# Optimization experiments

Hardware: AMD Instinct MI355X
Metric: run time of the kernel (lower is better)

The kernel has to match this reference:

```python
import jax, jax.numpy as jnp
import numpy as np

E, H = 1024, 16
N, S, T = 2, 2048, 2048


def setup_inputs() -> dict:
    key = jax.random.key(0)
    ks = jax.random.split(key, 8)
    scale = 1.0 / np.sqrt(E)
    q = jax.random.normal(ks[0], (N, S, E), dtype=jnp.float32)
    k = jax.random.normal(ks[1], (N, T, E), dtype=jnp.float32)
    v = jax.random.normal(ks[2], (N, T, E), dtype=jnp.float32)
    pad_mask = jax.random.randint(ks[3], (N, 1, 1, T), 0, 2, dtype=jnp.int32)
    subsq_mask = jnp.tril(jnp.ones((S, T), dtype=jnp.int32))[None, None]
    Wq = jax.random.normal(ks[4], (E, E), dtype=jnp.float32) * scale
    Wk = jax.random.normal(ks[5], (E, E), dtype=jnp.float32) * scale
    Wv = jax.random.normal(ks[6], (E, E), dtype=jnp.float32) * scale
    bq = jnp.zeros((E,), dtype=jnp.float32)
    bk = jnp.zeros((E,), dtype=jnp.float32)
    bv = jnp.zeros((E,), dtype=jnp.float32)
    return {"query": q, "key": k, "value": v, "pad_mask": pad_mask,
            "subsq_mask": subsq_mask, "Wq": Wq, "bq": bq, "Wk": Wk,
            "bk": bk, "Wv": Wv, "bv": bv}


def reference(query, key, value, pad_mask, subsq_mask, Wq, bq, Wk, bk, Wv, bv):
    n, s, e = query.shape
    t = value.shape[1]
    d = e // H
    # Linear projections (torch Linear: x @ W^T + b), split into heads
    q = (query @ Wq.T + bq).reshape(n, s, H, d).transpose(0, 2, 1, 3)  # [N,H,S,D]
    k = (key @ Wk.T + bk).reshape(n, t, H, d).transpose(0, 2, 1, 3)    # [N,H,T,D]
    v = (value @ Wv.T + bv).reshape(n, t, H, d).transpose(0, 2, 1, 3)  # [N,H,T,D]
    att = jnp.einsum('bhsd,bhtd->bhst', q, k) / jnp.sqrt(jnp.float32(d))
    att = jnp.where(pad_mask == 0, jnp.float32(-1e9), att)
    att = jnp.where(subsq_mask == 0, jnp.float32(-1e9), att)
    prob = jax.nn.softmax(att, axis=-1)
    out = jnp.einsum('bhst,bhtd->bhsd', prob, v)  # [N,H,S,D]
    return out.transpose(0, 2, 1, 3).reshape(n, s, e)
```

## Files before the change

kernel.cpp:

```cpp
#include <hip/hip_runtime.h>

#define HEADS 16
#define DH    64
#define EMB   1024
#define NBAT  2
#define SEQ   2048
#define KDIM  1024
#define NROW  (NBAT * SEQ)

typedef __attribute__((ext_vector_type(8))) short short8;
typedef __attribute__((ext_vector_type(4))) short short4v;
typedef __attribute__((ext_vector_type(4))) float floatx4;
typedef unsigned short u16;
typedef unsigned int   u32;
typedef unsigned long long u64;

__device__ __forceinline__ u16 f2bf(float x) {
    u32 u = __builtin_bit_cast(u32, x);
    u += 0x7fffu + ((u >> 16) & 1u);
    return (u16)(u >> 16);
}
__device__ __forceinline__ float bf2f(u16 v) {
    return __builtin_bit_cast(float, ((u32)v) << 16);
}

__device__ __forceinline__ void gll16(const u16* g, u16* l) {
    __builtin_amdgcn_global_load_lds((const __attribute__((address_space(1))) u32*)g,
                                     (__attribute__((address_space(3))) u32*)l, 16, 0, 0);
}

__global__ __launch_bounds__(256) void cvt_kernel(
    const float* __restrict__ q, const float* __restrict__ k, const float* __restrict__ v,
    const float* __restrict__ wq, const float* __restrict__ wk, const float* __restrict__ wv,
    u16* __restrict__ xb, u16* __restrict__ wb, float* __restrict__ vmean)
{
    const int z = blockIdx.y;
    if (z == 5 && blockIdx.x == 0) {
        for (int i = threadIdx.x; i < NBAT * HEADS * DH; i += 256) vmean[i] = 0.f;
    }
    const float* src; u16* dst; int n;
    if (z < 3) { src = (z == 0) ? q : (z == 1) ? k : v;     dst = xb + (size_t)z * 4194304;       n = 4194304; }
    else       { src = (z == 3) ? wq : (z == 4) ? wk : wv;  dst = wb + (size_t)(z - 3) * 1048576; n = 1048576; }
    for (int i = (blockIdx.x * 256 + threadIdx.x) * 8; i < n; i += 512 * 256 * 8) {
        float4 a = *(const float4*)(src + i);
        float4 b = *(const float4*)(src + i + 4);
        short8 o;
        o[0] = (short)f2bf(a.x); o[1] = (short)f2bf(a.y); o[2] = (short)f2bf(a.z); o[3] = (short)f2bf(a.w);
        o[4] = (short)f2bf(b.x); o[5] = (short)f2bf(b.y); o[6] = (short)f2bf(b.z); o[7] = (short)f2bf(b.w);
        *(short8*)(dst + i) = o;
    }
}

__global__ __launch_bounds__(256) void proj_kernel(
    const u16* __restrict__ xb, const u16* __restrict__ wb,
    const float* __restrict__ bq, const float* __restrict__ bk, const float* __restrict__ bv,
    u16* __restrict__ qh, u16* __restrict__ kh, u16* __restrict__ vt,
    float* __restrict__ vmean)
{
    const int f = blockIdx.x;
    const int xcd = f & 7, jj = f >> 3;
    const int g  = xcd * 12 + (jj >> 3);
    const int nx = jj & 7;
    const int z  = g >> 5, y = g & 31;

    const u16* A  = xb + (size_t)z * 4194304;
    const u16* B  = wb + (size_t)z * 1048576;
    const float* Bp = (z == 0) ? bq : (z == 1) ? bk : bv;
    u16* dst        = (z == 0) ? qh : (z == 1) ? kh : vt;

    const int m0 = y * 128;
    const int n0 = nx * 128;
    const int tid  = threadIdx.x;
    const int wave = tid >> 6, lane = tid & 63;
    const int quad = lane >> 4, l15 = lane & 15;
    const int waveM = wave >> 1, waveN = wave & 1;
    const int sw = l15 & 7;

    __shared__ __align__(16) u16 smem[2 * 128 * 64];
    u16* As = smem;
    u16* Bs = smem + 128 * 64;

    floatx4 acc[4][4];
    for (int a = 0; a < 4; a++)
        for (int b = 0; b < 4; b++)
            acc[a][b] = floatx4{0.f, 0.f, 0.f, 0.f};

    const int lrow = lane >> 3;
    const int gcol = ((lane & 7) ^ lrow) * 8;

    for (int k0 = 0; k0 < KDIM; k0 += 64) {
        for (int j = 0; j < 4; j++) {
            int r8 = wave * 32 + j * 8;
            gll16(A + (size_t)(m0 + r8 + lrow) * KDIM + k0 + gcol, &As[r8 * 64]);
        }
        for (int j = 0; j < 4; j++) {
            int r8 = wave * 32 + j * 8;
            gll16(B + (size_t)(n0 + r8 + lrow) * KDIM + k0 + gcol, &Bs[r8 * 64]);
        }
        __syncthreads();

        for (int ks = 0; ks < 2; ks++) {
            short8 af[4], bfg[4];
            for (int mb = 0; mb < 4; mb++)
                af[mb]  = *(const short8*)&As[(waveM * 64 + mb * 16 + l15) * 64 + ((ks * 4 + quad) ^ sw) * 8];
            for (int nb = 0; nb < 4; nb++)
                bfg[nb] = *(const short8*)&Bs[(waveN * 64 + nb * 16 + l15) * 64 + ((ks * 4 + quad) ^ sw) * 8];
            for (int mb = 0; mb < 4; mb++)
                for (int nb = 0; nb < 4; nb++)
                    acc[mb][nb] = __builtin_amdgcn_mfma_f32_16x16x32_bf16(af[mb], bfg[nb], acc[mb][nb], 0, 0, 0);
        }
        __syncthreads();
    }

    if (z != 2) {
        const int row0 = m0 + waveM * 64;
        const int col0 = n0 + waveN * 64;
        const float scale = (z == 0) ? 0.125f * 1.44269504f : 1.0f;
        for (int nb = 0; nb < 4; nb++) {
            int col = col0 + nb * 16 + l15;
            float bias = Bp[col];
            int hh = col >> 6, dd = col & 63;
            for (int mb = 0; mb < 4; mb++) {
                for (int r = 0; r < 4; r++) {
                    int row = row0 + mb * 16 + quad * 4 + r;
                    int nn = row >> 11, ss = row & 2047;
                    dst[((size_t)(nn * HEADS + hh) * SEQ + ss) * DH + dd] =
                        f2bf((acc[mb][nb][r] + bias) * scale);
                }
            }
        }
    } else {
        const int nn  = m0 >> 11;
        const int ss0 = m0 & 2047;
        for (int p = 0; p < 2; p++) {
            if (waveN == p) {
                float psum[4] = {0.f, 0.f, 0.f, 0.f};
                for (int nb = 0; nb < 4; nb++) {
                    int col_l = nb * 16 + l15;
                    float bias = Bp[n0 + p * 64 + col_l];
                    for (int mb = 0; mb < 4; mb++) {
                        short4v pk;
                        for (int r = 0; r < 4; r++) {
                            float vv = acc[mb][nb][r] + bias;
                            pk[r] = (short)f2bf(vv);
                            psum[nb] += vv;
                        }
                        *(short4v*)&smem[col_l * 136 + waveM * 64 + mb * 16 + quad * 4] = pk;
                    }
                }
                const int hh = (n0 >> 6) + p;
                for (int nb = 0; nb < 4; nb++) {
                    float s = psum[nb];
                    s += __shfl_xor(s, 16, 64);
                    s += __shfl_xor(s, 32, 64);
                    if (quad == 0)
                        atomicAdd(&vmean[(nn * HEADS + hh) * DH + nb * 16 + l15], s);
                }
            }
            __syncthreads();
            const int hh = (n0 >> 6) + p;
            u16* drow = dst + ((size_t)(nn * HEADS + hh) * DH) * SEQ + ss0;
            for (int c2 = tid; c2 < 1024; c2 += 256) {
                int dl = c2 >> 4, tc = (c2 & 15) * 8;
                short8 vv = *(const short8*)&smem[dl * 136 + tc];
                *(short8*)(drow + (size_t)dl * SEQ + tc) = vv;
            }
            __syncthreads();
        }
    }
}

__global__ __launch_bounds__(256) void attn_kernel(
    const u16* __restrict__ qh, const u16* __restrict__ kh, const u16* __restrict__ vt,
    const int* __restrict__ pad, const float* __restrict__ vmean,
    float* __restrict__ out)
{
    const int f = blockIdx.x;
    const int xcd = f & 7, jj = f >> 3;
    const int nh = xcd * 4 + (jj >> 4);
    const int pr = jj & 15;
    const int n = nh >> 4, h = nh & 15;
    const int tid  = threadIdx.x;
    const int wave = tid >> 6, lane = tid & 63;
    const int quad = lane >> 4, l15 = lane & 15;
    const int sw = l15 & 7;

    __shared__ __align__(16) u16 Ks[2][64 * 64];
    __shared__ __align__(16) u16 Vs[2][64 * 64];
    __shared__ __align__(16) u16 Ps[64 * 72];
    __shared__ u64 padb[32];

    {
        const int* pp = pad + n * SEQ;
        for (int i = 0; i < 8; i++) {
            int seg = wave * 8 + i;
            u64 m = __ballot(pp[seg * 64 + lane] != 0);
            if (lane == 0) padb[seg] = m;
        }
    }

    const u16* qbase = qh + (size_t)nh * SEQ * DH;
    const u16* kbase = kh + (size_t)nh * SEQ * DH;
    const u16* vbase = vt + (size_t)nh * DH * SEQ;

    short8 ones;
    for (int i = 0; i < 8; i++) ones[i] = (short)0x3F80;
    float vm[4];
    for (int nd = 0; nd < 4; nd++)
        vm[nd] = vmean[nh * DH + nd * 16 + l15] * (1.f / (float)SEQ);

    const int lrow = lane >> 3;
    const int gcol = ((lane & 7) ^ lrow) * 8;

    for (int half = 0; half < 2; half++) {
        const int sb = half ? (31 - pr) : pr;
        const int s0 = sb * 64;
        const int nt = sb + 1;
        const int srow = s0 + wave * 16 + l15;

        short8 qf[2];
        for (int ks = 0; ks < 2; ks++)
            qf[ks] = *(const short8*)(qbase + (size_t)srow * DH + ks * 32 + quad * 8);

        floatx4 oacc[4], lacc;
        for (int nd = 0; nd < 4; nd++) oacc[nd] = floatx4{0.f, 0.f, 0.f, 0.f};
        lacc = floatx4{0.f, 0.f, 0.f, 0.f};

        __syncthreads();

        for (int j = 0; j < 2; j++) {
            int r8 = wave * 16 + j * 8;
            gll16(kbase + (size_t)(r8 + lrow) * DH + gcol, &Ks[0][r8 * 64]);
            gll16(vbase + (size_t)(r8 + lrow) * SEQ + gcol, &Vs[0][r8 * 64]);
        }

        for (int tb = 0; tb < nt; tb++) {
            const int cur = tb & 1;
            __syncthreads();

            if (tb + 1 < nt) {
                const int t0n = (tb + 1) * 64;
                for (int j = 0; j < 2; j++) {
                    int r8 = wave * 16 + j * 8;
                    gll16(kbase + (size_t)(t0n + r8 + lrow) * DH + gcol, &Ks[1 - cur][r8 * 64]);
                    gll16(vbase + (size_t)(r8 + lrow) * SEQ + t0n + gcol, &Vs[1 - cur][r8 * 64]);
                }
            }

            const int t0 = tb * 64;
            const u64 w = padb[t0 >> 6];
            const bool diag = (tb == sb);

            floatx4 sc[4];
            for (int nb = 0; nb < 4; nb++) sc[nb] = floatx4{0.f, 0.f, 0.f, 0.f};
            __builtin_amdgcn_s_setprio(1);
            for (int ks = 0; ks < 2; ks++)
                for (int nb = 0; nb < 4; nb++) {
                    short8 kf = *(const short8*)&Ks[cur][(nb * 16 + l15) * 64 + ((ks * 4 + quad) ^ sw) * 8];
                    sc[nb] = __builtin_amdgcn_mfma_f32_16x16x32_bf16(kf, qf[ks], sc[nb], 0, 0, 0);
                }
            __builtin_amdgcn_s_setprio(0);

            for (int nb = 0; nb < 4; nb++) {
                short4v pk;
                for (int r = 0; r < 4; r++) {
                    int sh = nb * 16 + quad * 4 + r;
                    bool ok = ((w >> sh) & 1ull) != 0;
                    if (diag) ok = ok && (t0 + sh <= srow);
                    float p = ok ? __builtin_amdgcn_exp2f(sc[nb][r]) : 0.f;
                    pk[r] = (short)f2bf(p);
                }
                *(short4v*)&Ps[(wave * 16 + l15) * 72 + nb * 16 + quad * 4] = pk;
            }
            asm volatile("s_waitcnt lgkmcnt(0)" ::: "memory");

            __builtin_amdgcn_s_setprio(1);
            for (int ks = 0; ks < 2; ks++) {
                short8 pa = *(const short8*)&Ps[(wave * 16 + l15) * 72 + ks * 32 + quad * 8];
                for (int nd = 0; nd < 4; nd++) {
                    short8 vb = *(const short8*)&Vs[cur][(nd * 16 + l15) * 64 + ((ks * 4 + quad) ^ sw) * 8];
                    oacc[nd] = __builtin_amdgcn_mfma_f32_16x16x32_bf16(pa, vb, oacc[nd], 0, 0, 0);
                }
                lacc = __builtin_amdgcn_mfma_f32_16x16x32_bf16(pa, ones, lacc, 0, 0, 0);
            }
            __builtin_amdgcn_s_setprio(0);
        }

        for (int r = 0; r < 4; r++) {
            float l = lacc[r];
            int s = s0 + wave * 16 + quad * 4 + r;
            float* orow = out + (size_t)(n * SEQ + s) * EMB + h * DH;
            if (l > 0.f) {
                float inv = 1.f / l;
                for (int nd = 0; nd < 4; nd++) orow[nd * 16 + l15] = oacc[nd][r] * inv;
            } else {
                for (int nd = 0; nd < 4; nd++) orow[nd * 16 + l15] = vm[nd];
            }
        }
    }
}

extern "C" void kernel_launch(void* const* d_in, const int* in_sizes, int n_in,
                              void* d_out, int out_size, void* d_ws, size_t ws_size,
                              hipStream_t stream)
{
    const float* qin = (const float*)d_in[0];
    const float* kin = (const float*)d_in[1];
    const float* vin = (const float*)d_in[2];
    const int*   pad = (const int*)d_in[3];
    const float* Wq = (const float*)d_in[5];
    const float* bq = (const float*)d_in[6];
    const float* Wk = (const float*)d_in[7];
    const float* bk = (const float*)d_in[8];
    const float* Wv = (const float*)d_in[9];
    const float* bv = (const float*)d_in[10];
    float* out = (float*)d_out;

    const size_t per = (size_t)NBAT * HEADS * SEQ * DH;
    u16* qh = (u16*)d_ws;
    u16* kh = qh + per;
    u16* vt = kh + per;
    float* vmean = (float*)(vt + per);
    u16* xb = (u16*)(vmean + 2048);
    u16* wb = xb + 3 * per;

    cvt_kernel<<<dim3(512, 6), 256, 0, stream>>>(qin, kin, vin, Wq, Wk, Wv, xb, wb, vmean);
    proj_kernel<<<dim3(768), 256, 0, stream>>>(xb, wb, bq, bk, bv, qh, kh, vt, vmean);
    attn_kernel<<<dim3(512), 256, 0, stream>>>(qh, kh, vt, pad, vmean, out);
}
```

Measured before the change: 214.5 us.

## Use four-slot K/V ring and process two tiles per barrier

Grows the shared K/V staging to four slots and prefetches two tiles ahead, so each barrier covers two 64-key tiles instead of one. This halves the number of __syncthreads in the attention loop and gives the async global loads more time to land. LDS use roughly doubles for K/V, which may reduce the number of resident blocks per CU.

```diff
diff --git a/kernel.cpp b/kernel.cpp
--- a/kernel.cpp
+++ b/kernel.cpp
@@ -185,8 +185,8 @@
     const int quad = lane >> 4, l15 = lane & 15;
     const int sw = l15 & 7;
 
-    __shared__ __align__(16) u16 Ks[2][64 * 64];
-    __shared__ __align__(16) u16 Vs[2][64 * 64];
+    __shared__ __align__(16) u16 Ks[4][64 * 64];
+    __shared__ __align__(16) u16 Vs[4][64 * 64];
     __shared__ __align__(16) u16 Ps[64 * 72];
     __shared__ u64 padb[32];
 
@@ -233,57 +233,76 @@
             gll16(kbase + (size_t)(r8 + lrow) * DH + gcol, &Ks[0][r8 * 64]);
             gll16(vbase + (size_t)(r8 + lrow) * SEQ + gcol, &Vs[0][r8 * 64]);
         }
-
-        for (int tb = 0; tb < nt; tb++) {
-            const int cur = tb & 1;
+        if (1 < nt) {
+            for (int j = 0; j < 2; j++) {
+                int r8 = wave * 16 + j * 8;
+                gll16(kbase + (size_t)(64 + r8 + lrow) * DH + gcol, &Ks[1][r8 * 64]);
+                gll16(vbase + (size_t)(r8 + lrow) * SEQ + 64 + gcol, &Vs[1][r8 * 64]);
+            }
+        }
+
+        for (int tb = 0; tb < nt; tb += 2) {
             __syncthreads();
 
-            if (tb + 1 < nt) {
-                const int t0n = (tb + 1) * 64;
+            if (tb + 2 < nt) {
+                const int t0n = (tb + 2) * 64, sl = (tb + 2) & 3;
                 for (int j = 0; j < 2; j++) {
                     int r8 = wave * 16 + j * 8;
-                    gll16(kbase + (size_t)(t0n + r8 + lrow) * DH + gcol, &Ks[1 - cur][r8 * 64]);
-                    gll16(vbase + (size_t)(r8 + lrow) * SEQ + t0n + gcol, &Vs[1 - cur][r8 * 64]);
-                }
-            }
-
-            const int t0 = tb * 64;
-            const u64 w = padb[t0 >> 6];
-            const bool diag = (tb == sb);
-
-            floatx4 sc[4];
-            for (int nb = 0; nb < 4; nb++) sc[nb] = floatx4{0.f, 0.f, 0.f, 0.f};
-            __builtin_amdgcn_s_setprio(1);
-            for (int ks = 0; ks < 2; ks++)
+                    gll16(kbase + (size_t)(t0n + r8 + lrow) * DH + gcol, &Ks[sl][r8 * 64]);
+                    gll16(vbase + (size_t)(r8 + lrow) * SEQ + t0n + gcol, &Vs[sl][r8 * 64]);
+                }
+            }
+            if (tb + 3 < nt) {
+                const int t0n = (tb + 3) * 64, sl = (tb + 3) & 3;
+                for (int j = 0; j < 2; j++) {
+                    int r8 = wave * 16 + j * 8;
+                    gll16(kbase + (size_t)(t0n + r8 + lrow) * DH + gcol, &Ks[sl][r8 * 64]);
+                    gll16(vbase + (size_t)(r8 + lrow) * SEQ + t0n + gcol, &Vs[sl][r8 * 64]);
+                }
+            }
+
+            for (int u = 0; u < 2; u++) {
+                const int tc = tb + u;
+                if (tc >= nt) break;
+                const int cur = tc & 3;
+                const int t0 = tc * 64;
+                const u64 w = padb[tc];
+                const bool diag = (tc == sb);
+
+                floatx4 sc[4];
+                for (int nb = 0; nb < 4; nb++) sc[nb] = floatx4{0.f, 0.f, 0.f, 0.f};
+                __builtin_amdgcn_s_setprio(1);
+                for (int ks = 0; ks < 2; ks++)
+                    for (int nb = 0; nb < 4; nb++) {
+                        short8 kf = *(const short8*)&Ks[cur][(nb * 16 + l15) * 64 + ((ks * 4 + quad) ^ sw) * 8];
+                        sc[nb] = __builtin_amdgcn_mfma_f32_16x16x32_bf16(kf, qf[ks], sc[nb], 0, 0, 0);
+                    }
+                __builtin_amdgcn_s_setprio(0);
+
                 for (int nb = 0; nb < 4; nb++) {
-                    short8 kf = *(const short8*)&Ks[cur][(nb * 16 + l15) * 64 + ((ks * 4 + quad) ^ sw) * 8];
-                    sc[nb] = __builtin_amdgcn_mfma_f32_16x16x32_bf16(kf, qf[ks], sc[nb], 0, 0, 0);
-                }
-            __builtin_amdgcn_s_setprio(0);
-
-            for (int nb = 0; nb < 4; nb++) {
-                short4v pk;
-                for (int r = 0; r < 4; r++) {
-                    int sh = nb * 16 + quad * 4 + r;
-                    bool ok = ((w >> sh) & 1ull) != 0;
-                    if (diag) ok = ok && (t0 + sh <= srow);
-                    float p = ok ? __builtin_amdgcn_exp2f(sc[nb][r]) : 0.f;
-                    pk[r] = (short)f2bf(p);
-                }
-                *(short4v*)&Ps[(wave * 16 + l15) * 72 + nb * 16 + quad * 4] = pk;
-            }
-            asm volatile("s_waitcnt lgkmcnt(0)" ::: "memory");
-
-            __builtin_amdgcn_s_setprio(1);
-            for (int ks = 0; ks < 2; ks++) {
-                short8 pa = *(const short8*)&Ps[(wave * 16 + l15) * 72 + ks * 32 + quad * 8];
-                for (int nd = 0; nd < 4; nd++) {
-                    short8 vb = *(const short8*)&Vs[cur][(nd * 16 + l15) * 64 + ((ks * 4 + quad) ^ sw) * 8];
-                    oacc[nd] = __builtin_amdgcn_mfma_f32_16x16x32_bf16(pa, vb, oacc[nd], 0, 0, 0);
-                }
-                lacc = __builtin_amdgcn_mfma_f32_16x16x32_bf16(pa, ones, lacc, 0, 0, 0);
-            }
-            __builtin_amdgcn_s_setprio(0);
+                    short4v pk;
+                    for (int r = 0; r < 4; r++) {
+                        int sh = nb * 16 + quad * 4 + r;
+                        bool ok = ((w >> sh) & 1ull) != 0;
+                        if (diag) ok = ok && (t0 + sh <= srow);
+                        float p = ok ? __builtin_amdgcn_exp2f(sc[nb][r]) : 0.f;
+                        pk[r] = (short)f2bf(p);
+                    }
+                    *(short4v*)&Ps[(wave * 16 + l15) * 72 + nb * 16 + quad * 4] = pk;
+                }
+                asm volatile("s_waitcnt lgkmcnt(0)" ::: "memory");
+
+                __builtin_amdgcn_s_setprio(1);
+                for (int ks = 0; ks < 2; ks++) {
+                    short8 pa = *(const short8*)&Ps[(wave * 16 + l15) * 72 + ks * 32 + quad * 8];
+                    for (int nd = 0; nd < 4; nd++) {
+                        short8 vb = *(const short8*)&Vs[cur][(nd * 16 + l15) * 64 + ((ks * 4 + quad) ^ sw) * 8];
+                        oacc[nd] = __builtin_amdgcn_mfma_f32_16x16x32_bf16(pa, vb, oacc[nd], 0, 0, 0);
+                    }
+                    lacc = __builtin_amdgcn_mfma_f32_16x16x32_bf16(pa, ones, lacc, 0, 0, 0);
+                }
+                __builtin_amdgcn_s_setprio(0);
+            }
         }
 
         for (int r = 0; r < 4; r++) {
```

Result: slower. 225.4 us (+5.1%).
